# Optimization experiments

Hardware: AMD Instinct MI355X
Metric: run time of the kernel (lower is better)

The kernel has to match this reference:

```python
import jax, jax.numpy as jnp
import numpy as np

EMBED_DIM = 1024
BATCH = 4
SEQ = 2048


def setup_inputs() -> dict:
    key = jax.random.key(0)
    ks = jax.random.split(key, 9)
    E = EMBED_DIM
    s = 1.0 / np.sqrt(E)
    inp = {
        "x": jax.random.normal(ks[0], (BATCH, SEQ, E), dtype=jnp.float32),
        "Wq": jax.random.uniform(ks[1], (E, E), jnp.float32, -s, s),
        "bq": jax.random.uniform(ks[2], (E,), jnp.float32, -s, s),
        "Wk": jax.random.uniform(ks[3], (E, E), jnp.float32, -s, s),
        "bk": jax.random.uniform(ks[4], (E,), jnp.float32, -s, s),
        "Wv": jax.random.uniform(ks[5], (E, E), jnp.float32, -s, s),
        "bv": jax.random.uniform(ks[6], (E,), jnp.float32, -s, s),
        "Wo": jax.random.uniform(ks[7], (E, E), jnp.float32, -s, s),
        "bo": jax.random.uniform(ks[8], (E,), jnp.float32, -s, s),
    }
    return inp


def reference(x, Wq, bq, Wk, bk, Wv, bv, Wo, bo):
    # x: [B, S, E]. Single-head attention over full embed_dim.
    scale = x.shape[-1] ** -0.5
    q = jnp.einsum("bse,ef->bsf", x, Wq.T) + bq
    k = jnp.einsum("bse,ef->bsf", x, Wk.T) + bk
    v = jnp.einsum("bse,ef->bsf", x, Wv.T) + bv
    scores = jnp.einsum("bqe,bke->bqk", q, k) * scale  # [B, S, S]
    attn = jax.nn.softmax(scores, axis=-1)             # dropout p=0 -> identity
    out = jnp.einsum("bqk,bke->bqe", attn, v)
    return jnp.einsum("bse,ef->bsf", out, Wo.T) + bo
```

## Files before the change

### kernel.cpp

```cpp
#include <hip/hip_runtime.h>
#include <hip/hip_bf16.h>


typedef __bf16 bf16_t;
typedef __bf16 bf16x8 __attribute__((ext_vector_type(8)));
typedef __bf16 bf16x4 __attribute__((ext_vector_type(4)));
typedef float  f32x16 __attribute__((ext_vector_type(16)));
typedef float  f32x4  __attribute__((ext_vector_type(4)));

__device__ __forceinline__ void async_copy16(const void* g, void* l) {
  __builtin_amdgcn_global_load_lds(
      (const __attribute__((address_space(1))) void*)g,
      (__attribute__((address_space(3))) void*)l, 16, 0, 0);
}

__device__ __forceinline__ void wg_barrier() {
  asm volatile("" ::: "memory");
  __builtin_amdgcn_s_barrier();
  asm volatile("" ::: "memory");
}

#define LGKM(n)                                                  \
  do {                                                           \
    asm volatile("s_waitcnt lgkmcnt(" #n ")" ::: "memory");      \
    __builtin_amdgcn_sched_barrier(0);                           \
  } while (0)

__device__ __forceinline__ unsigned lds_addr(const void* p) {
  return (unsigned)(unsigned long long)(__attribute__((address_space(3))) const void*)p;
}

__device__ __forceinline__ bf16x8 ds_read128(const bf16_t* p) {
  bf16x8 r;
  asm volatile("ds_read_b128 %0, %1" : "=v"(r) : "v"(lds_addr(p)));
  return r;
}

__device__ __forceinline__ f32x4 mfma16(bf16x8 a, bf16x8 b, f32x4 c) {
  return __builtin_amdgcn_mfma_f32_16x16x32_bf16(a, b, c, 0, 0, 0);
}

__device__ __forceinline__ void store_out(float* p, float v)  { *p = v; }
__device__ __forceinline__ void store_out(bf16_t* p, float v) { *p = (bf16_t)v; }

#define BM 128
#define BN 128
#define BKT 64

#define G_AQ(i, ro, bb, co)                                                   \
  acc[(ro) + (i)][(co) + 0] = mfma16(a[i][0], bb[0][0], acc[(ro) + (i)][(co) + 0]); \
  acc[(ro) + (i)][(co) + 1] = mfma16(a[i][0], bb[1][0], acc[(ro) + (i)][(co) + 1]); \
  acc[(ro) + (i)][(co) + 0] = mfma16(a[i][1], bb[0][1], acc[(ro) + (i)][(co) + 0]); \
  acc[(ro) + (i)][(co) + 1] = mfma16(a[i][1], bb[1][1], acc[(ro) + (i)][(co) + 1]);

#define G_BQ(j, bb, co)                                              \
  acc[0][(co) + (j)] = mfma16(a[0][0], bb[j][0], acc[0][(co) + (j)]); \
  acc[1][(co) + (j)] = mfma16(a[1][0], bb[j][0], acc[1][(co) + (j)]); \
  acc[2][(co) + (j)] = mfma16(a[2][0], bb[j][0], acc[2][(co) + (j)]); \
  acc[3][(co) + (j)] = mfma16(a[3][0], bb[j][0], acc[3][(co) + (j)]); \
  acc[0][(co) + (j)] = mfma16(a[0][1], bb[j][1], acc[0][(co) + (j)]); \
  acc[1][(co) + (j)] = mfma16(a[1][1], bb[j][1], acc[1][(co) + (j)]); \
  acc[2][(co) + (j)] = mfma16(a[2][1], bb[j][1], acc[2][(co) + (j)]); \
  acc[3][(co) + (j)] = mfma16(a[3][1], bb[j][1], acc[3][(co) + (j)]);

template <typename OutT, int NBIAS>
__global__ __launch_bounds__(512, 2) void gemm256_bt(
    const bf16_t* __restrict__ A, const bf16_t* __restrict__ B,
    OutT* __restrict__ C,
    const float* __restrict__ b0, const float* __restrict__ b1,
    const float* __restrict__ b2,
    int M, int N, int K, int lda, int ldb, int ldc, float scale,
    long long strideA, long long strideB, long long strideC) {
  const int z = blockIdx.z;
  A += (long long)z * strideA;
  B += (long long)z * strideB;
  C += (long long)z * strideC;

  int bx = blockIdx.x, by = blockIdx.y;
  {
    const int GX  = gridDim.x;
    const int id  = by * GX + bx;
    const int per = GX * 8;
    const int grp = id / per;
    const int rem = id - grp * per;
    by = grp * 8 + (rem & 7);
    bx = rem >> 3;
  }

  __shared__ __align__(16) bf16_t As[2 * 256 * 64];
  __shared__ __align__(16) bf16_t Bs[2 * 256 * 64];

  const int t    = threadIdx.x;
  const int lane = t & 63;
  const int w    = t >> 6;
  const int wm   = w & 1;
  const int wn   = w >> 1;
  const int g    = lane >> 4;
  const int l7   = lane & 7;
  const int r15  = lane & 15;
  const int tileM = by * 256;
  const int tileN = bx * 256;

  const int row0 = t >> 3;
  const int gcc  = (t & 7) ^ (row0 & 7);
  const int dstb = (t & ~63) * 8;

  const int sw0 = ((0 + g) ^ l7) * 8;
  const int sw1 = ((4 + g) ^ l7) * 8;
  const int aRow = (wm * 128 + r15) * 64;
  const int bRow = (wn * 64 + r15) * 64;

  const int NT = K >> 6;

  f32x4 acc[8][4] = {};

  auto stageA = [&](int kt, int h) {
    const int cb = (kt & 1) * 16384;
    const bf16_t* src =
        A + (long long)(tileM + h * 128 + row0) * lda + kt * 64 + gcc * 8;
    bf16_t* dst = &As[cb + h * 8192 + dstb];
    async_copy16(src, dst);
    async_copy16(src + (long long)64 * lda, dst + 4096);
  };
  auto stageB = [&](int kt, int h) {
    const int cb = (kt & 1) * 16384;
    const bf16_t* src =
        B + (long long)(tileN + h * 128 + row0) * ldb + kt * 64 + gcc * 8;
    bf16_t* dst = &Bs[cb + h * 8192 + dstb];
    async_copy16(src, dst);
    async_copy16(src + (long long)64 * ldb, dst + 4096);
  };

  stageA(0, 0); stageA(0, 1); stageB(0, 0); stageB(0, 1);
  asm volatile("s_waitcnt vmcnt(0)" ::: "memory");
  wg_barrier();

  bf16x8 a[4][2], P[2][2], Q[2][2];
#pragma unroll
  for (int j = 0; j < 2; ++j) {
    P[j][0] = ds_read128(&Bs[bRow + j * 1024 + sw0]);
    P[j][1] = ds_read128(&Bs[bRow + j * 1024 + sw1]);
  }

  auto tile_step = [&](int kt, bf16x8 (&bc)[2][2], bf16x8 (&bq)[2][2]) {
    const int cb = (kt & 1) * 16384;
    const int kn = kt + 1;
    const bf16_t* Ab = &As[cb + aRow];
    const bf16_t* Bb = &Bs[cb + bRow];

#pragma unroll
    for (int i = 0; i < 4; ++i) {
      a[i][0] = ds_read128(Ab + i * 1024 + sw0);
      a[i][1] = ds_read128(Ab + i * 1024 + sw1);
    }
    if (kn < NT) { stageB(kn, 0); stageB(kn, 1); }
    __builtin_amdgcn_s_setprio(1);
    LGKM(6);
    G_AQ(0, 0, bc, 0)
    LGKM(4);
    G_AQ(1, 0, bc, 0)
    LGKM(2);
    G_AQ(2, 0, bc, 0)
    LGKM(0);
    G_AQ(3, 0, bc, 0)
    __builtin_amdgcn_s_setprio(0);

#pragma unroll
    for (int j = 0; j < 2; ++j) {
      bq[j][0] = ds_read128(Bb + 2048 + j * 1024 + sw0);
      bq[j][1] = ds_read128(Bb + 2048 + j * 1024 + sw1);
    }
    if (kn < NT) { stageA(kn, 0); stageA(kn, 1); }
    __builtin_amdgcn_s_setprio(1);
    LGKM(2);
    G_BQ(0, bq, 2)
    LGKM(0);
    G_BQ(1, bq, 2)
    __builtin_amdgcn_s_setprio(0);

#pragma unroll
    for (int i = 0; i < 4; ++i) {
      a[i][0] = ds_read128(Ab + 4096 + i * 1024 + sw0);
      a[i][1] = ds_read128(Ab + 4096 + i * 1024 + sw1);
    }
    __builtin_amdgcn_s_setprio(1);
    LGKM(6);
    G_AQ(0, 4, bq, 2)
    LGKM(4);
    G_AQ(1, 4, bq, 2)
    LGKM(2);
    G_AQ(2, 4, bq, 2)
    LGKM(0);
    G_AQ(3, 4, bq, 2)
    __builtin_amdgcn_s_setprio(0);
    asm volatile("s_waitcnt vmcnt(0)" ::: "memory");
    wg_barrier();

    if (kn < NT) {
      const bf16_t* Bn = &Bs[(kn & 1) * 16384 + bRow];
#pragma unroll
      for (int j = 0; j < 2; ++j) {
        bq[j][0] = ds_read128(Bn + j * 1024 + sw0);
        bq[j][1] = ds_read128(Bn + j * 1024 + sw1);
      }
    }
    __builtin_amdgcn_s_setprio(1);
    G_AQ(0, 4, bc, 0)
    G_AQ(1, 4, bc, 0)
    G_AQ(2, 4, bc, 0)
    G_AQ(3, 4, bc, 0)
    __builtin_amdgcn_s_setprio(0);
  };

  for (int kt = 0; kt < NT; kt += 2) {
    tile_step(kt,     P, Q);
    tile_step(kt + 1, Q, P);
  }

  float bvv[4];
#pragma unroll
  for (int j = 0; j < 4; ++j) {
    const int col = tileN + wn * 64 + j * 16 + r15;
    float bv = 0.f;
    if (NBIAS == 1) bv = b0[col];
    if (NBIAS == 3) {
      const float* bp = col < 1024 ? b0 : (col < 2048 ? b1 : b2);
      bv = bp[col & 1023];
    }
    bvv[j] = bv;
  }
#pragma unroll
  for (int i = 0; i < 8; ++i) {
#pragma unroll
    for (int r = 0; r < 4; ++r) {
      const long long row = tileM + wm * 128 + i * 16 + g * 4 + r;
      OutT* Crow = C + row * ldc + tileN + wn * 64 + r15;
#pragma unroll
      for (int j = 0; j < 4; ++j)
        store_out(Crow + j * 16, acc[i][j][r] * scale + bvv[j]);
    }
  }
}

template <typename OutT, int NBIAS>
__global__ __launch_bounds__(256) void gemm_bt(
    const bf16_t* __restrict__ A, const bf16_t* __restrict__ B,
    OutT* __restrict__ C,
    const float* __restrict__ b0, const float* __restrict__ b1,
    const float* __restrict__ b2,
    int M, int N, int K, int lda, int ldb, int ldc, float scale,
    long long strideA, long long strideB, long long strideC) {
  const int z = blockIdx.z;
  A += (long long)z * strideA;
  B += (long long)z * strideB;
  C += (long long)z * strideC;

  int bx = blockIdx.x, by = blockIdx.y;
  {
    const int GX  = gridDim.x;
    const int id  = by * GX + bx;
    const int per = GX * 8;
    const int grp = id / per;
    const int rem = id - grp * per;
    by = grp * 8 + (rem & 7);
    bx = rem >> 3;
  }

  __shared__ __align__(16) bf16_t As[BM * BKT];
  __shared__ __align__(16) bf16_t Bs[BN * BKT];

  const int t    = threadIdx.x;
  const int lane = t & 63;
  const int w    = t >> 6;
  const int wm   = w & 1;
  const int wn   = w >> 1;
  const int tileM = by * BM;
  const int tileN = bx * BN;

  f32x16 acc[2][2] = {};

  for (int k0 = 0; k0 < K; k0 += BKT) {
#pragma unroll
    for (int i = 0; i < 4; ++i) {
      const int c   = t + 256 * i;
      const int row = c >> 3;
      const int cc  = c & 7;
      const int gcc = cc ^ (row & 7);
      const int ldsbase = ((t & ~63) + 256 * i) * 8;
      async_copy16(A + (long long)(tileM + row) * lda + k0 + gcc * 8, &As[ldsbase]);
      async_copy16(B + (long long)(tileN + row) * ldb + k0 + gcc * 8, &Bs[ldsbase]);
    }
    __syncthreads();

#pragma unroll
    for (int s = 0; s < 4; ++s) {
      const int kc = s + 4 * (lane >> 5);
      bf16x8 af[2], bfr[2];
#pragma unroll
      for (int ti = 0; ti < 2; ++ti) {
        const int row = wm * 64 + ti * 32 + (lane & 31);
        af[ti] = *(const bf16x8*)&As[row * BKT + ((kc ^ (row & 7)) * 8)];
      }
#pragma unroll
      for (int tj = 0; tj < 2; ++tj) {
        const int row = wn * 64 + tj * 32 + (lane & 31);
        bfr[tj] = *(const bf16x8*)&Bs[row * BKT + ((kc ^ (row & 7)) * 8)];
      }
#pragma unroll
      for (int ti = 0; ti < 2; ++ti)
#pragma unroll
        for (int tj = 0; tj < 2; ++tj)
          acc[ti][tj] = __builtin_amdgcn_mfma_f32_32x32x16_bf16(
              af[ti], bfr[tj], acc[ti][tj], 0, 0, 0);
    }
    __syncthreads();
  }

#pragma unroll
  for (int tj = 0; tj < 2; ++tj) {
    const int col = tileN + wn * 64 + tj * 32 + (lane & 31);
    float bv = 0.f;
    if (NBIAS == 1) bv = b0[col];
    if (NBIAS == 3) {
      const float* bp = col < 1024 ? b0 : (col < 2048 ? b1 : b2);
      bv = bp[col & 1023];
    }
#pragma unroll
    for (int ti = 0; ti < 2; ++ti) {
      const int rowb = tileM + wm * 64 + ti * 32 + 4 * (lane >> 5);
#pragma unroll
      for (int r = 0; r < 16; ++r) {
        const int row = rowb + (r & 3) + 8 * (r >> 2);
        store_out(&C[(long long)row * ldc + col], acc[ti][tj][r] * scale + bv);
      }
    }
  }
}

__global__ __launch_bounds__(256) void cast_all(
    const float4* __restrict__ w0, const float4* __restrict__ w1,
    const float4* __restrict__ w2, const float4* __restrict__ w3,
    const float4* __restrict__ x,
    bf16x4* __restrict__ wdst, bf16x4* __restrict__ xdst) {
  const int N4W = 1 << 18;
  const int id = blockIdx.x * 256 + threadIdx.x;
  const float4* src;
  bf16x4* dst;
  if (id < 4 * N4W) {
    const int z = id >> 18;
    src = (z == 0 ? w0 : z == 1 ? w1 : z == 2 ? w2 : w3) + (id & (N4W - 1));
    dst = wdst + id;
  } else {
    const int i = id - 4 * N4W;
    src = x + i;
    dst = xdst + i;
  }
  const float4 v = *src;
  bf16x4 o;
  o[0] = (bf16_t)v.x; o[1] = (bf16_t)v.y; o[2] = (bf16_t)v.z; o[3] = (bf16_t)v.w;
  *dst = o;
}

__global__ __launch_bounds__(256) void transpose_bf16(
    const bf16_t* __restrict__ in, bf16_t* __restrict__ out, int R, int C,
    int ldin, long long sIn, long long sOut) {
  in  += (long long)blockIdx.z * sIn;
  out += (long long)blockIdx.z * sOut;
  __shared__ bf16_t tile[32][33];
  const int tx = threadIdx.x, ty = threadIdx.y;
  const int x = blockIdx.x * 32 + tx;
  const int y0 = blockIdx.y * 32;
#pragma unroll
  for (int j = 0; j < 32; j += 8)
    tile[ty + j][tx] = in[(long long)(y0 + ty + j) * ldin + x];
  __syncthreads();
  const int x2 = y0 + tx;
  const int y2 = blockIdx.x * 32;
#pragma unroll
  for (int j = 0; j < 32; j += 8)
    out[(long long)(y2 + ty + j) * R + x2] = tile[tx][ty + j];
}

__global__ __launch_bounds__(256) void softmax_rows(
    const bf16_t* __restrict__ S, bf16_t* __restrict__ P, int cols) {
  const long long row = blockIdx.x;
  const bf16x8* inp = (const bf16x8*)(S + row * cols);
  bf16x8* outp      = (bf16x8*)(P + row * cols);
  const int t = threadIdx.x;
  const int w = t >> 6, lane = t & 63;

  const bf16x8 v = inp[t];
  float f[8];
#pragma unroll
  for (int j = 0; j < 8; ++j) f[j] = (float)v[j];

  float m = f[0];
#pragma unroll
  for (int j = 1; j < 8; ++j) m = fmaxf(m, f[j]);
#pragma unroll
  for (int off = 32; off > 0; off >>= 1) m = fmaxf(m, __shfl_xor(m, off));

  __shared__ float red[8];
  if (lane == 0) red[w] = m;
  __syncthreads();
  m = fmaxf(fmaxf(red[0], red[1]), fmaxf(red[2], red[3]));

  float e[8], sum = 0.f;
#pragma unroll
  for (int j = 0; j < 8; ++j) { e[j] = __expf(f[j] - m); sum += e[j]; }
#pragma unroll
  for (int off = 32; off > 0; off >>= 1) sum += __shfl_xor(sum, off);
  if (lane == 0) red[4 + w] = sum;
  __syncthreads();
  sum = red[4] + red[5] + red[6] + red[7];

  const float inv = 1.f / sum;
  bf16x8 o;
#pragma unroll
  for (int j = 0; j < 8; ++j) o[j] = (bf16_t)(e[j] * inv);
  outp[t] = o;
}

extern "C" void kernel_launch(void* const* d_in, const int* in_sizes, int n_in,
                              void* d_out, int out_size, void* d_ws, size_t ws_size,
                              hipStream_t stream) {
  const int E = 1024, S = 2048, B = 4;
  const int BS = B * S;

  const float* x  = (const float*)d_in[0];
  const float* Wq = (const float*)d_in[1];
  const float* bq = (const float*)d_in[2];
  const float* Wk = (const float*)d_in[3];
  const float* bk = (const float*)d_in[4];
  const float* Wv = (const float*)d_in[5];
  const float* bv = (const float*)d_in[6];
  const float* Wo = (const float*)d_in[7];
  const float* bo = (const float*)d_in[8];
  float* out = (float*)d_out;

  char* w = (char*)d_ws;
  const size_t MB = 1ull << 20;
  bf16_t* Wqkvb = (bf16_t*)(w + 0 * MB);
  bf16_t* Wob   = Wqkvb + 3 * E * E;
  bf16_t* xb    = (bf16_t*)(w + 8 * MB);
  bf16_t* QKVb  = (bf16_t*)(w + 24 * MB);
  bf16_t* VTb   = (bf16_t*)(w + 72 * MB);
  bf16_t* Sb    = (bf16_t*)(w + 88 * MB);
  bf16_t* Pb    = (bf16_t*)(w + 8 * MB);
  bf16_t* Ob    = (bf16_t*)(w + 40 * MB);

  {
    const int totalBlocks = ((4 << 18) + (1 << 21)) / 256;
    cast_all<<<totalBlocks, 256, 0, stream>>>(
        (const float4*)Wq, (const float4*)Wk, (const float4*)Wv,
        (const float4*)Wo, (const float4*)x, (bf16x4*)Wqkvb, (bf16x4*)xb);
  }

  gemm256_bt<bf16_t, 3><<<dim3(3 * E / 256, BS / 256, 1), 512, 0, stream>>>(
      xb, Wqkvb, QKVb, bq, bk, bv,
      BS, 3 * E, E, E, E, 3 * E, 1.f, 0, 0, 0);

  transpose_bf16<<<dim3(E / 32, S / 32, B), dim3(32, 8), 0, stream>>>(
      QKVb + 2 * E, VTb, S, E, 3 * E, (long long)S * 3 * E, (long long)E * S);

  gemm256_bt<bf16_t, 0><<<dim3(S / 256, S / 256, B), 512, 0, stream>>>(
      QKVb, QKVb + E, Sb, nullptr, nullptr, nullptr,
      S, S, E, 3 * E, 3 * E, S, 0.03125f,
      (long long)S * 3 * E, (long long)S * 3 * E, (long long)S * S);

  softmax_rows<<<BS, 256, 0, stream>>>(Sb, Pb, S);

  gemm_bt<bf16_t, 0><<<dim3(E / BN, S / BM, B), 256, 0, stream>>>(
      Pb, VTb, Ob, nullptr, nullptr, nullptr,
      S, E, S, S, S, E, 1.f,
      (long long)S * S, (long long)E * S, (long long)S * E);

  gemm_bt<float, 1><<<dim3(E / BN, BS / BM, 1), 256, 0, stream>>>(
      Ob, Wob, out, bo, nullptr, nullptr,
      BS, E, E, E, E, E, 1.f, 0, 0, 0);
}
```

Measured before the change: 287.1 us.

## Fold K projection into Q via Wq^T Wk product, dropping K GEMM

Rewrites the scores as x·(Wq^T Wk)·x^T plus a per-column bias term bq·Wk, so the K projection is never materialized and the QKV projection shrinks to two outputs. A small E×E GEMM computes the combined weight and a tiny kernel computes the bias vector. Terms that are constant per query row (those involving bk) are dropped because softmax is invariant to them. This removes one third of the projection GEMM and its stores at the cost of extra weight transposes and an E×E GEMM, plus a change in bf16 rounding because the combined matrix is rounded separately.

```diff
diff --git a/kernel.cpp b/kernel.cpp
--- a/kernel.cpp
+++ b/kernel.cpp
@@ -25,6 +25,8 @@
     asm volatile("s_waitcnt lgkmcnt(" #n ")" ::: "memory");      \
     __builtin_amdgcn_sched_barrier(0);                           \
   } while (0)
+
+#define VM(n) asm volatile("s_waitcnt vmcnt(" #n ")" ::: "memory")
 
 __device__ __forceinline__ unsigned lds_addr(const void* p) {
   return (unsigned)(unsigned long long)(__attribute__((address_space(3))) const void*)p;
@@ -132,7 +134,7 @@
   };
 
   stageA(0, 0); stageA(0, 1); stageB(0, 0); stageB(0, 1);
-  asm volatile("s_waitcnt vmcnt(0)" ::: "memory");
+  VM(0);
   wg_barrier();
 
   bf16x8 a[4][2], P[2][2], Q[2][2];
@@ -193,7 +195,7 @@
     LGKM(0);
     G_AQ(3, 4, bq, 2)
     __builtin_amdgcn_s_setprio(0);
-    asm volatile("s_waitcnt vmcnt(0)" ::: "memory");
+    VM(0);
     wg_barrier();
 
     if (kn < NT) {
@@ -341,15 +343,18 @@
     const float4* __restrict__ w0, const float4* __restrict__ w1,
     const float4* __restrict__ w2, const float4* __restrict__ w3,
     const float4* __restrict__ x,
-    bf16x4* __restrict__ wdst, bf16x4* __restrict__ xdst) {
+    bf16x4* __restrict__ d0, bf16x4* __restrict__ d1,
+    bf16x4* __restrict__ d2, bf16x4* __restrict__ d3,
+    bf16x4* __restrict__ xdst) {
   const int N4W = 1 << 18;
   const int id = blockIdx.x * 256 + threadIdx.x;
   const float4* src;
   bf16x4* dst;
   if (id < 4 * N4W) {
     const int z = id >> 18;
-    src = (z == 0 ? w0 : z == 1 ? w1 : z == 2 ? w2 : w3) + (id & (N4W - 1));
-    dst = wdst + id;
+    const int i = id & (N4W - 1);
+    src = (z == 0 ? w0 : z == 1 ? w1 : z == 2 ? w2 : w3) + i;
+    dst = (z == 0 ? d0 : z == 1 ? d1 : z == 2 ? d2 : d3) + i;
   } else {
     const int i = id - 4 * N4W;
     src = x + i;
@@ -359,6 +364,16 @@
   bf16x4 o;
   o[0] = (bf16_t)v.x; o[1] = (bf16_t)v.y; o[2] = (bf16_t)v.z; o[3] = (bf16_t)v.w;
   *dst = o;
+}
+
+__global__ __launch_bounds__(256) void bias_v(
+    const float* __restrict__ Wk, const float* __restrict__ bq,
+    float* __restrict__ v) {
+  const int j = blockIdx.x * 256 + threadIdx.x;
+  float acc = 0.f;
+#pragma unroll 4
+  for (int c = 0; c < 1024; ++c) acc += bq[c] * Wk[c * 1024 + j];
+  v[j] = acc;
 }
 
 __global__ __launch_bounds__(256) void transpose_bf16(
@@ -437,36 +452,53 @@
   const float* Wo = (const float*)d_in[7];
   const float* bo = (const float*)d_in[8];
   float* out = (float*)d_out;
+  (void)bk;
 
   char* w = (char*)d_ws;
   const size_t MB = 1ull << 20;
-  bf16_t* Wqkvb = (bf16_t*)(w + 0 * MB);
-  bf16_t* Wob   = Wqkvb + 3 * E * E;
-  bf16_t* xb    = (bf16_t*)(w + 8 * MB);
-  bf16_t* QKVb  = (bf16_t*)(w + 24 * MB);
-  bf16_t* VTb   = (bf16_t*)(w + 72 * MB);
-  bf16_t* Sb    = (bf16_t*)(w + 88 * MB);
-  bf16_t* Pb    = (bf16_t*)(w + 8 * MB);
-  bf16_t* Ob    = (bf16_t*)(w + 40 * MB);
+  bf16_t* Wqb  = (bf16_t*)(w + 0 * MB);
+  bf16_t* Wkb  = Wqb + E * E;
+  bf16_t* Wob  = (bf16_t*)(w + 4 * MB);
+  float*  vb   = (float*)(w + 6 * MB);
+  bf16_t* xb   = (bf16_t*)(w + 8 * MB);
+  bf16_t* QVb  = (bf16_t*)(w + 24 * MB);
+  bf16_t* WqTb = (bf16_t*)(w + 56 * MB);
+  bf16_t* WkTb = WqTb + E * E;
+  bf16_t* Wqv  = (bf16_t*)(w + 60 * MB);
+  bf16_t* Wvb  = Wqv + E * E;
+  bf16_t* VTb  = (bf16_t*)(w + 72 * MB);
+  bf16_t* Sb   = (bf16_t*)(w + 88 * MB);
+  bf16_t* Pb   = (bf16_t*)(w + 8 * MB);
+  bf16_t* Ob   = (bf16_t*)(w + 40 * MB);
 
   {
     const int totalBlocks = ((4 << 18) + (1 << 21)) / 256;
     cast_all<<<totalBlocks, 256, 0, stream>>>(
         (const float4*)Wq, (const float4*)Wk, (const float4*)Wv,
-        (const float4*)Wo, (const float4*)x, (bf16x4*)Wqkvb, (bf16x4*)xb);
-  }
-
-  gemm256_bt<bf16_t, 3><<<dim3(3 * E / 256, BS / 256, 1), 512, 0, stream>>>(
-      xb, Wqkvb, QKVb, bq, bk, bv,
-      BS, 3 * E, E, E, E, 3 * E, 1.f, 0, 0, 0);
+        (const float4*)Wo, (const float4*)x,
+        (bf16x4*)Wqb, (bf16x4*)Wkb, (bf16x4*)Wvb, (bf16x4*)Wob, (bf16x4*)xb);
+  }
+
+  transpose_bf16<<<dim3(E / 32, E / 32, 2), dim3(32, 8), 0, stream>>>(
+      Wqb, WqTb, E, E, E, (long long)E * E, (long long)E * E);
+
+  bias_v<<<4, 256, 0, stream>>>(Wk, bq, vb);
+
+  gemm_bt<bf16_t, 0><<<dim3(E / BN, E / BM, 1), 256, 0, stream>>>(
+      WkTb, WqTb, Wqv, nullptr, nullptr, nullptr,
+      E, E, E, E, E, E, 1.f, 0, 0, 0);
+
+  gemm256_bt<bf16_t, 3><<<dim3(2 * E / 256, BS / 256, 1), 512, 0, stream>>>(
+      xb, Wqv, QVb, vb, bv, bv,
+      BS, 2 * E, E, E, E, 2 * E, 1.f, 0, 0, 0);
 
   transpose_bf16<<<dim3(E / 32, S / 32, B), dim3(32, 8), 0, stream>>>(
-      QKVb + 2 * E, VTb, S, E, 3 * E, (long long)S * 3 * E, (long long)E * S);
+      QVb + E, VTb, S, E, 2 * E, (long long)S * 2 * E, (long long)E * S);
 
   gemm256_bt<bf16_t, 0><<<dim3(S / 256, S / 256, B), 512, 0, stream>>>(
-      QKVb, QKVb + E, Sb, nullptr, nullptr, nullptr,
-      S, S, E, 3 * E, 3 * E, S, 0.03125f,
-      (long long)S * 3 * E, (long long)S * 3 * E, (long long)S * S);
+      QVb, xb, Sb, nullptr, nullptr, nullptr,
+      S, S, E, 2 * E, E, S, 0.03125f,
+      (long long)S * 2 * E, (long long)S * E, (long long)S * S);
 
   softmax_rows<<<BS, 256, 0, stream>>>(Sb, Pb, S);
 
```

New measurement: 376.0 us. 31.0% more time.
